# Optimization experiments

Measured on AMD Instinct MI355X. Metric: run time of the kernel, lower is better.

The kernel has to match this reference:

```python
import jax, jax.numpy as jnp
import numpy as np

M_DIM = 1024
N_HEADS = 16
H_DIM = M_DIM // N_HEADS
FFN_H = 2 * M_DIM
B, S = 2, 2048
EPS = 1e-5
NEG = -1e9


def layernorm(x, g, b):
    mu = jnp.mean(x, axis=-1, keepdims=True)
    var = jnp.mean((x - mu) ** 2, axis=-1, keepdims=True)
    return (x - mu) * jax.lax.rsqrt(var + EPS) * g + b


def setup_inputs() -> dict:
    key = jax.random.key(0)
    ks = jax.random.split(key, 16)
    sc = 0.02
    return {
        "x": jax.random.normal(ks[0], (B, S, M_DIM), jnp.float32),
        "attention_mask": jnp.ones((B, S), jnp.int32),
        # per-head QKV projections stacked over heads: [H, M, D]
        "Wq": jax.random.normal(ks[1], (N_HEADS, M_DIM, H_DIM), jnp.float32) * sc,
        "bq": jnp.zeros((N_HEADS, H_DIM), jnp.float32),
        "Wk": jax.random.normal(ks[2], (N_HEADS, M_DIM, H_DIM), jnp.float32) * sc,
        "bk": jnp.zeros((N_HEADS, H_DIM), jnp.float32),
        "Wv": jax.random.normal(ks[3], (N_HEADS, M_DIM, H_DIM), jnp.float32) * sc,
        "bv": jnp.zeros((N_HEADS, H_DIM), jnp.float32),
        "Wo": jax.random.normal(ks[4], (M_DIM, M_DIM), jnp.float32) * sc,
        "bo": jnp.zeros((M_DIM,), jnp.float32),
        "g1": jnp.ones((M_DIM,), jnp.float32),
        "b1": jnp.zeros((M_DIM,), jnp.float32),
        "W1": jax.random.normal(ks[5], (M_DIM, FFN_H), jnp.float32) * sc,
        "bias1": jnp.zeros((FFN_H,), jnp.float32),
        "W2": jax.random.normal(ks[6], (FFN_H, M_DIM), jnp.float32) * sc,
        "bias2": jnp.zeros((M_DIM,), jnp.float32),
        "g2": jnp.ones((M_DIM,), jnp.float32),
        "b2": jnp.zeros((M_DIM,), jnp.float32),
    }


def reference(x, attention_mask, Wq, bq, Wk, bk, Wv, bv, Wo, bo, g1, b1, W1, bias1, W2, bias2, g2, b2):
    # All heads at once (the torch code loops over heads; same math).
    q = jnp.einsum("bsm,hmd->bhsd", x, Wq) + bq[None, :, None, :]
    k = jnp.einsum("bsm,hmd->bhsd", x, Wk) + bk[None, :, None, :]
    v = jnp.einsum("bsm,hmd->bhsd", x, Wv) + bv[None, :, None, :]
    scores = jnp.einsum("bhqd,bhkd->bhqk", q, k) / jnp.sqrt(jnp.float32(H_DIM))
    mask = attention_mask[:, None, None, :].astype(bool)  # [B,1,1,S] over keys
    scores = jnp.where(mask, scores, NEG)
    attn = jax.nn.softmax(scores, axis=-1)
    ctx = jnp.einsum("bhqk,bhkd->bhqd", attn, v)
    ctx = ctx.transpose(0, 2, 1, 3).reshape(x.shape[0], x.shape[1], M_DIM)  # concat heads
    out = ctx @ Wo + bo
    out = layernorm(out + x, g1, b1)
    fout = jax.nn.relu(out @ W1 + bias1) @ W2 + bias2
    out = layernorm(out + fout, g2, b2)
    return out
```

## Files before the change

kernel.cpp:

```cpp
#include <hip/hip_runtime.h>

#define MDIM 1024
#define FFH  2048
#define SEQ  2048
#define AST  72
#define VST  136
#define QSCL 0.18033688f

#if __has_builtin(__builtin_amdgcn_exp2f)
  #define EXP2(x) __builtin_amdgcn_exp2f(x)
#else
  #define EXP2(x) exp2f(x)
#endif

typedef __attribute__((ext_vector_type(8))) __bf16 bf16x8;
typedef __attribute__((ext_vector_type(4))) float floatx4;
typedef __attribute__((ext_vector_type(8))) unsigned short ushort8;
typedef __attribute__((address_space(3))) unsigned int lds_uint;
typedef const __attribute__((address_space(1))) unsigned int g_uint;

__device__ __forceinline__ unsigned short f2bf(float f){
  union { float f; unsigned u; } v; v.f = f;
  unsigned u = v.u;
  u += 0x7fffu + ((u >> 16) & 1u);
  return (unsigned short)(u >> 16);
}
__device__ __forceinline__ unsigned short f2bf_tr(float f){
  union { float f; unsigned u; } v; v.f = f;
  return (unsigned short)(v.u >> 16);
}

__global__ void k_cvt_qb(const float* __restrict__ x, unsigned short* __restrict__ xb,
                         const float* __restrict__ bq, const float* __restrict__ bk,
                         const float* __restrict__ bv, float* __restrict__ qbias){
  const int bid = blockIdx.x, t = threadIdx.x;
  if (bid < 4096){
    int i = (bid * 256 + t) * 4;
    float4 v = *(const float4*)(x + i);
    ushort4 o;
    o.x = f2bf(v.x); o.y = f2bf(v.y); o.z = f2bf(v.z); o.w = f2bf(v.w);
    *(ushort4*)(xb + i) = o;
  } else {
    int i = (bid - 4096) * 256 + t;
    qbias[i] = (i < 1024) ? bq[i] * QSCL : (i < 2048) ? bk[i - 1024] : bv[i - 2048];
  }
}

__global__ void __launch_bounds__(256) k_prep_w(const float* __restrict__ Wo, const float* __restrict__ W1,
                                                const float* __restrict__ W2, const float* __restrict__ Wq,
                                                const float* __restrict__ Wk, const float* __restrict__ Wv,
                                                unsigned short* __restrict__ wot, unsigned short* __restrict__ w1t,
                                                unsigned short* __restrict__ w2t, unsigned short* __restrict__ wqkvt){
  __shared__ unsigned short Ts[32 * 36];
  const int t = threadIdx.x, bid = blockIdx.x;
  const int lr = t >> 3, lc4 = (t & 7) << 2;
  if (bid >= 5120){
    const int id = bid - 5120;
    const int xm = id & 31, yd = (id >> 5) & 1, z = id >> 6;
    const int tensor = z >> 4, h = z & 15;
    const float* W = (tensor == 0) ? Wq : (tensor == 1) ? Wk : Wv;
    const float scl = (tensor == 0) ? QSCL : 1.0f;
    const int m0 = xm << 5, d0 = yd << 5;
    float4 v = *(const float4*)(W + ((size_t)h << 16) + (size_t)(m0 + lr) * 64 + d0 + lc4);
    ushort4 o; o.x = f2bf(v.x * scl); o.y = f2bf(v.y * scl); o.z = f2bf(v.z * scl); o.w = f2bf(v.w * scl);
    *(ushort4*)&Ts[lr * 36 + lc4] = o;
    __syncthreads();
    ushort4 w;
    w.x = Ts[(lc4 + 0) * 36 + lr];
    w.y = Ts[(lc4 + 1) * 36 + lr];
    w.z = Ts[(lc4 + 2) * 36 + lr];
    w.w = Ts[(lc4 + 3) * 36 + lr];
    const int n = (tensor << 10) + (h << 6) + d0 + lr;
    *(ushort4*)(wqkvt + ((size_t)n << 10) + m0 + lc4) = w;
    return;
  }
  const float* src; unsigned short* dst; int K, N, k0, n0;
  if (bid < 1024){
    src = Wo; dst = wot; K = 1024; N = 1024;
    n0 = (bid & 31) << 5; k0 = (bid >> 5) << 5;
  } else if (bid < 3072){
    const int id = bid - 1024;
    src = W1; dst = w1t; K = 1024; N = 2048;
    n0 = (id & 63) << 5; k0 = (id >> 6) << 5;
  } else {
    const int id = bid - 3072;
    src = W2; dst = w2t; K = 2048; N = 1024;
    n0 = (id & 31) << 5; k0 = (id >> 5) << 5;
  }
  float4 v = *(const float4*)(src + (size_t)(k0 + lr) * N + n0 + lc4);
  ushort4 o; o.x = f2bf(v.x); o.y = f2bf(v.y); o.z = f2bf(v.z); o.w = f2bf(v.w);
  *(ushort4*)&Ts[lr * 36 + lc4] = o;
  __syncthreads();
  ushort4 w;
  w.x = Ts[(lc4 + 0) * 36 + lr];
  w.y = Ts[(lc4 + 1) * 36 + lr];
  w.z = Ts[(lc4 + 2) * 36 + lr];
  w.w = Ts[(lc4 + 3) * 36 + lr];
  *(ushort4*)(dst + (size_t)(n0 + lr) * K + k0 + lc4) = w;
}

template<int RELU, int OUTBF>
__global__ void __launch_bounds__(256) k_gemm128(const unsigned short* __restrict__ A,
                                                 const unsigned short* __restrict__ Bt,
                                                 const float* __restrict__ bias,
                                                 void* __restrict__ Cout, int N, int K){
  __shared__ unsigned short As[2][2 * 128 * 32];
  __shared__ unsigned short Bs[2][2 * 128 * 32];
  const int t = threadIdx.x;
  const int m0 = blockIdx.y << 7, n0 = blockIdx.x << 7;
  const int lane = t & 63, w = t >> 6;
  const int quad = lane >> 4, l16 = lane & 15;
  const int mw = (w & 1) << 6, nw = (w >> 1) << 6;
  floatx4 acc[4][4];
  #pragma unroll
  for (int i = 0; i < 4; i++)
    #pragma unroll
    for (int j = 0; j < 4; j++) acc[i][j] = (floatx4){0.f, 0.f, 0.f, 0.f};
  const unsigned short* Ag  = A  + (size_t)(m0 + (t >> 2)) * K + ((t & 3) << 3);
  const unsigned short* Ag2 = Ag + (size_t)64 * K;
  const unsigned short* Bg  = Bt + (size_t)(n0 + (t >> 2)) * K + ((t & 3) << 3);
  const unsigned short* Bg2 = Bg + (size_t)64 * K;

#define STG128(Ad, Bd, kb) { \
    _Pragma("unroll") \
    for (int s = 0; s < 2; s++){ \
      const int ko = (kb) + (s << 5), lo = (s << 12) + (t << 3); \
      __builtin_amdgcn_global_load_lds((g_uint*)(Ag  + ko), (lds_uint*)&(Ad)[lo],        16, 0, 0); \
      __builtin_amdgcn_global_load_lds((g_uint*)(Ag2 + ko), (lds_uint*)&(Ad)[lo + 2048], 16, 0, 0); \
      __builtin_amdgcn_global_load_lds((g_uint*)(Bg  + ko), (lds_uint*)&(Bd)[lo],        16, 0, 0); \
      __builtin_amdgcn_global_load_lds((g_uint*)(Bg2 + ko), (lds_uint*)&(Bd)[lo + 2048], 16, 0, 0); \
    } }

  STG128(As[0], Bs[0], 0);
  __syncthreads();
  int cur = 0;
  for (int kb = 0; kb < K; kb += 64){
    if (kb + 64 < K) STG128(As[cur ^ 1], Bs[cur ^ 1], kb + 64);
    const unsigned short* Ar = As[cur];
    const unsigned short* Br = Bs[cur];
    #pragma unroll
    for (int s = 0; s < 2; s++){
      const int sb = s << 12;
      bf16x8 af[4], bf[4];
      #pragma unroll
      for (int mt = 0; mt < 4; mt++)
        af[mt] = *(const bf16x8*)&Ar[sb + ((mw + (mt << 4) + l16) << 5) + (quad << 3)];
      #pragma unroll
      for (int nt = 0; nt < 4; nt++)
        bf[nt] = *(const bf16x8*)&Br[sb + ((nw + (nt << 4) + l16) << 5) + (quad << 3)];
      #pragma unroll
      for (int mt = 0; mt < 4; mt++)
        #pragma unroll
        for (int nt = 0; nt < 4; nt++)
          acc[mt][nt] = __builtin_amdgcn_mfma_f32_16x16x32_bf16(af[mt], bf[nt], acc[mt][nt], 0, 0, 0);
    }
    __syncthreads();
    cur ^= 1;
  }
#undef STG128
  #pragma unroll
  for (int nt = 0; nt < 4; nt++){
    const int col = n0 + nw + (nt << 4) + l16;
    const float bsv = bias[col];
    #pragma unroll
    for (int mt = 0; mt < 4; mt++){
      const int row = m0 + mw + (mt << 4) + (quad << 2);
      #pragma unroll
      for (int r = 0; r < 4; r++){
        float v = acc[mt][nt][r] + bsv;
        if (RELU) v = fmaxf(v, 0.f);
        if (OUTBF) ((unsigned short*)Cout)[(size_t)(row + r) * N + col] = f2bf(v);
        else       ((float*)Cout)[(size_t)(row + r) * N + col] = v;
      }
    }
  }
}

template<int RELU, int OUTBF>
__global__ void __launch_bounds__(256) k_gemm64n(const unsigned short* __restrict__ A,
                                                 const unsigned short* __restrict__ Bt,
                                                 const float* __restrict__ bias,
                                                 void* __restrict__ Cout, int N, int K){
  __shared__ unsigned short As[2][2 * 128 * 32];
  __shared__ unsigned short Bs[2][2 * 64 * 32];
  const int t = threadIdx.x;
  const int m0 = blockIdx.y << 7, n0 = blockIdx.x << 6;
  const int lane = t & 63, w = t >> 6;
  const int quad = lane >> 4, l16 = lane & 15;
  const int mw = (w & 1) << 6, nw = (w >> 1) << 5;
  floatx4 acc[4][2];
  #pragma unroll
  for (int i = 0; i < 4; i++)
    #pragma unroll
    for (int j = 0; j < 2; j++) acc[i][j] = (floatx4){0.f, 0.f, 0.f, 0.f};
  const unsigned short* Ag  = A  + (size_t)(m0 + (t >> 2)) * K + ((t & 3) << 3);
  const unsigned short* Ag2 = Ag + (size_t)64 * K;
  const unsigned short* Bg  = Bt + (size_t)(n0 + (t >> 2)) * K + ((t & 3) << 3);

#define STG64(Ad, Bd, kb) { \
    _Pragma("unroll") \
    for (int s = 0; s < 2; s++){ \
      const int ko = (kb) + (s << 5); \
      __builtin_amdgcn_global_load_lds((g_uint*)(Ag  + ko), (lds_uint*)&(Ad)[(s << 12) + (t << 3)],        16, 0, 0); \
      __builtin_amdgcn_global_load_lds((g_uint*)(Ag2 + ko), (lds_uint*)&(Ad)[(s << 12) + (t << 3) + 2048], 16, 0, 0); \
      __builtin_amdgcn_global_load_lds((g_uint*)(Bg  + ko), (lds_uint*)&(Bd)[(s << 11) + (t << 3)],        16, 0, 0); \
    } }

  STG64(As[0], Bs[0], 0);
  __syncthreads();
  int cur = 0;
  for (int kb = 0; kb < K; kb += 64){
    if (kb + 64 < K) STG64(As[cur ^ 1], Bs[cur ^ 1], kb + 64);
    const unsigned short* Ar = As[cur];
    const unsigned short* Br = Bs[cur];
    #pragma unroll
    for (int s = 0; s < 2; s++){
      bf16x8 af[4], bf[2];
      #pragma unroll
      for (int mt = 0; mt < 4; mt++)
        af[mt] = *(const bf16x8*)&Ar[(s << 12) + ((mw + (mt << 4) + l16) << 5) + (quad << 3)];
      #pragma unroll
      for (int nt = 0; nt < 2; nt++)
        bf[nt] = *(const bf16x8*)&Br[(s << 11) + ((nw + (nt << 4) + l16) << 5) + (quad << 3)];
      #pragma unroll
      for (int mt = 0; mt < 4; mt++)
        #pragma unroll
        for (int nt = 0; nt < 2; nt++)
          acc[mt][nt] = __builtin_amdgcn_mfma_f32_16x16x32_bf16(af[mt], bf[nt], acc[mt][nt], 0, 0, 0);
    }
    __syncthreads();
    cur ^= 1;
  }
#undef STG64
  #pragma unroll
  for (int nt = 0; nt < 2; nt++){
    const int col = n0 + nw + (nt << 4) + l16;
    const float bsv = bias[col];
    #pragma unroll
    for (int mt = 0; mt < 4; mt++){
      const int row = m0 + mw + (mt << 4) + (quad << 2);
      #pragma unroll
      for (int r = 0; r < 4; r++){
        float v = acc[mt][nt][r] + bsv;
        if (RELU) v = fmaxf(v, 0.f);
        if (OUTBF) ((unsigned short*)Cout)[(size_t)(row + r) * N + col] = f2bf(v);
        else       ((float*)Cout)[(size_t)(row + r) * N + col] = v;
      }
    }
  }
}

__global__ void __launch_bounds__(256, 2) k_attn(const unsigned short* __restrict__ qkvb,
                                                 const int* __restrict__ amask,
                                                 unsigned short* __restrict__ ctxb){
  __shared__ __align__(16) unsigned short Ks[2][128 * AST];
  __shared__ __align__(16) unsigned short Vt[2][64 * VST];
  __shared__ __align__(16) int msk[2][128];
  const int t = threadIdx.x;
  const int w = t >> 6, lane = t & 63;
  const int quad = lane >> 4, l16 = lane & 15;
  const int b = blockIdx.y >> 4, h = blockIdx.y & 15;
  const int q0 = blockIdx.x << 7;
  const int r0 = (w << 5) + l16;
  const int r1 = r0 + 16;
  const int sr = t >> 2, sc = (t & 3) << 4;
  const int kg = t >> 4, dc = (t & 15) << 2;
  const int swz  = (dc >> 4) & 3;
  const int pc0  = ((((kg & 3) | ((kg >> 3) << 2)) ^ swz) << 3) | (((kg >> 2) & 1) << 2);

  {
    const int qr = t >> 1, qc = (t & 1) << 5;
    const unsigned short* qs = qkvb + (size_t)((b << 11) + q0 + qr) * 3072 + (h << 6) + qc;
    unsigned short* qd = &Ks[0][qr * AST + qc];
    *(uint4*)(qd)      = *(const uint4*)(qs);
    *(uint4*)(qd + 8)  = *(const uint4*)(qs + 8);
    *(uint4*)(qd + 16) = *(const uint4*)(qs + 16);
    *(uint4*)(qd + 24) = *(const uint4*)(qs + 24);
  }
  __syncthreads();
  const bf16x8 qa0 = *(const bf16x8*)&Ks[0][r0 * AST + (quad << 3)];
  const bf16x8 qa1 = *(const bf16x8*)&Ks[0][r0 * AST + (quad << 3) + 32];
  const bf16x8 qb0 = *(const bf16x8*)&Ks[0][r1 * AST + (quad << 3)];
  const bf16x8 qb1 = *(const bf16x8*)&Ks[0][r1 * AST + (quad << 3) + 32];

  floatx4 accA[4], accB[4];
  #pragma unroll
  for (int i = 0; i < 4; i++){
    accA[i] = (floatx4){0.f, 0.f, 0.f, 0.f};
    accB[i] = (floatx4){0.f, 0.f, 0.f, 0.f};
  }
  float l_runA = 0.f, l_runB = 0.f;

  const unsigned short* kbase  = qkvb + (size_t)((b << 11) + sr) * 3072 + 1024 + (h << 6) + sc;
  const unsigned short* kbase2 = kbase + (size_t)64 * 3072;
  const unsigned short* vbase  = qkvb + (size_t)((b << 11) + (kg << 2)) * 3072 + 2048 + (h << 6) + dc;
  const unsigned short* vbase2 = vbase + (size_t)64 * 3072;
  const int* mbase = amask + (b << 11);

  uint4 krA, krB, krC, krD;
  ushort4 va0, va1, va2, va3, vb0, vb1, vb2, vb3;
  int mreg = 1;

#define LOADT(tt) { \
    const size_t off = (size_t)((tt) << 7) * 3072; \
    krA = *(const uint4*)(kbase + off); \
    krB = *(const uint4*)(kbase + off + 8); \
    krC = *(const uint4*)(kbase2 + off); \
    krD = *(const uint4*)(kbase2 + off + 8); \
    va0 = *(const ushort4*)(vbase + off); \
    va1 = *(const ushort4*)(vbase + off + 3072); \
    va2 = *(const ushort4*)(vbase + off + 2 * 3072); \
    va3 = *(const ushort4*)(vbase + off + 3 * 3072); \
    vb0 = *(const ushort4*)(vbase2 + off); \
    vb1 = *(const ushort4*)(vbase2 + off + 3072); \
    vb2 = *(const ushort4*)(vbase2 + off + 2 * 3072); \
    vb3 = *(const ushort4*)(vbase2 + off + 3 * 3072); \
    if (t < 128) mreg = mbase[((tt) << 7) + t]; \
  }

#define STORET(dst) { \
    unsigned short* Kd = Ks[dst]; \
    unsigned short* Vd = Vt[dst]; \
    *(uint4*)&Kd[sr * AST + sc]            = krA; \
    *(uint4*)&Kd[sr * AST + sc + 8]        = krB; \
    *(uint4*)&Kd[(sr + 64) * AST + sc]     = krC; \
    *(uint4*)&Kd[(sr + 64) * AST + sc + 8] = krD; \
    ushort4 cc; \
    cc.x = va0.x; cc.y = va1.x; cc.z = va2.x; cc.w = va3.x; *(ushort4*)&Vd[(dc + 0) * VST + pc0] = cc; \
    cc.x = va0.y; cc.y = va1.y; cc.z = va2.y; cc.w = va3.y; *(ushort4*)&Vd[(dc + 1) * VST + pc0] = cc; \
    cc.x = va0.z; cc.y = va1.z; cc.z = va2.z; cc.w = va3.z; *(ushort4*)&Vd[(dc + 2) * VST + pc0] = cc; \
    cc.x = va0.w; cc.y = va1.w; cc.z = va2.w; cc.w = va3.w; *(ushort4*)&Vd[(dc + 3) * VST + pc0] = cc; \
    cc.x = vb0.x; cc.y = vb1.x; cc.z = vb2.x; cc.w = vb3.x; *(ushort4*)&Vd[(dc + 0) * VST + pc0 + 64] = cc; \
    cc.x = vb0.y; cc.y = vb1.y; cc.z = vb2.y; cc.w = vb3.y; *(ushort4*)&Vd[(dc + 1) * VST + pc0 + 64] = cc; \
    cc.x = vb0.z; cc.y = vb1.z; cc.z = vb2.z; cc.w = vb3.z; *(ushort4*)&Vd[(dc + 2) * VST + pc0 + 64] = cc; \
    cc.x = vb0.w; cc.y = vb1.w; cc.z = vb2.w; cc.w = vb3.w; *(ushort4*)&Vd[(dc + 3) * VST + pc0 + 64] = cc; \
    if (t < 128) msk[dst][t] = mreg; \
  }

  LOADT(0);
  __syncthreads();
  STORET(0);
  LOADT(1);
  __syncthreads();

  int c = 0;
  for (int kt = 0; kt < 16; kt++){
    if (kt + 1 < 16) STORET(c ^ 1);
    if (kt + 2 < 16) LOADT(kt + 2);
    {
      const unsigned short* Kc = Ks[c];
      const unsigned short* Vc = Vt[c];
      const int* Mc = msk[c];
      float lsA = 0.f, lsB = 0.f;
      #pragma unroll
      for (int s = 0; s < 4; s++){
        const unsigned short* kp = &Kc[((s << 5) + l16) * AST + (quad << 3)];
        const bf16x8 k00 = *(const bf16x8*)(kp);
        const bf16x8 k01 = *(const bf16x8*)(kp + 32);
        const bf16x8 k10 = *(const bf16x8*)(kp + (AST << 4));
        const bf16x8 k11 = *(const bf16x8*)(kp + (AST << 4) + 32);
        floatx4 sA0 = (floatx4){0.f, 0.f, 0.f, 0.f};
        floatx4 sB0 = (floatx4){0.f, 0.f, 0.f, 0.f};
        floatx4 sA1 = (floatx4){0.f, 0.f, 0.f, 0.f};
        floatx4 sB1 = (floatx4){0.f, 0.f, 0.f, 0.f};
        __builtin_amdgcn_s_setprio(1);
        sA0 = __builtin_amdgcn_mfma_f32_16x16x32_bf16(k00, qa0, sA0, 0, 0, 0);
        sA0 = __builtin_amdgcn_mfma_f32_16x16x32_bf16(k01, qa1, sA0, 0, 0, 0);
        sB0 = __builtin_amdgcn_mfma_f32_16x16x32_bf16(k00, qb0, sB0, 0, 0, 0);
        sB0 = __builtin_amdgcn_mfma_f32_16x16x32_bf16(k01, qb1, sB0, 0, 0, 0);
        sA1 = __builtin_amdgcn_mfma_f32_16x16x32_bf16(k10, qa0, sA1, 0, 0, 0);
        sA1 = __builtin_amdgcn_mfma_f32_16x16x32_bf16(k11, qa1, sA1, 0, 0, 0);
        sB1 = __builtin_amdgcn_mfma_f32_16x16x32_bf16(k10, qb0, sB1, 0, 0, 0);
        sB1 = __builtin_amdgcn_mfma_f32_16x16x32_bf16(k11, qb1, sB1, 0, 0, 0);
        __builtin_amdgcn_s_setprio(0);
        const int4 m0 = *(const int4*)&Mc[(s << 5) + (quad << 2)];
        const int4 m1 = *(const int4*)&Mc[(s << 5) + 16 + (quad << 2)];
        const float a0 = m0.x ? EXP2(sA0[0]) : 0.f;
        const float a1 = m0.y ? EXP2(sA0[1]) : 0.f;
        const float a2 = m0.z ? EXP2(sA0[2]) : 0.f;
        const float a3 = m0.w ? EXP2(sA0[3]) : 0.f;
        const float a4 = m1.x ? EXP2(sA1[0]) : 0.f;
        const float a5 = m1.y ? EXP2(sA1[1]) : 0.f;
        const float a6 = m1.z ? EXP2(sA1[2]) : 0.f;
        const float a7 = m1.w ? EXP2(sA1[3]) : 0.f;
        const float b0 = m0.x ? EXP2(sB0[0]) : 0.f;
        const float b1 = m0.y ? EXP2(sB0[1]) : 0.f;
        const float b2 = m0.z ? EXP2(sB0[2]) : 0.f;
        const float b3 = m0.w ? EXP2(sB0[3]) : 0.f;
        const float b4 = m1.x ? EXP2(sB1[0]) : 0.f;
        const float b5 = m1.y ? EXP2(sB1[1]) : 0.f;
        const float b6 = m1.z ? EXP2(sB1[2]) : 0.f;
        const float b7 = m1.w ? EXP2(sB1[3]) : 0.f;
        lsA += (a0 + a1) + (a2 + a3) + (a4 + a5) + (a6 + a7);
        lsB += (b0 + b1) + (b2 + b3) + (b4 + b5) + (b6 + b7);
        ushort8 uA, uB;
        uA[0] = f2bf_tr(a0); uA[1] = f2bf_tr(a1); uA[2] = f2bf_tr(a2); uA[3] = f2bf_tr(a3);
        uA[4] = f2bf_tr(a4); uA[5] = f2bf_tr(a5); uA[6] = f2bf_tr(a6); uA[7] = f2bf_tr(a7);
        uB[0] = f2bf_tr(b0); uB[1] = f2bf_tr(b1); uB[2] = f2bf_tr(b2); uB[3] = f2bf_tr(b3);
        uB[4] = f2bf_tr(b4); uB[5] = f2bf_tr(b5); uB[6] = f2bf_tr(b6); uB[7] = f2bf_tr(b7);
        const bf16x8 pfA = __builtin_bit_cast(bf16x8, uA);
        const bf16x8 pfB = __builtin_bit_cast(bf16x8, uB);
        __builtin_amdgcn_s_setprio(1);
        #pragma unroll
        for (int mt = 0; mt < 4; mt++){
          const bf16x8 vf = *(const bf16x8*)&Vc[((mt << 4) + l16) * VST + ((((s << 2) + quad) ^ mt) << 3)];
          accA[mt] = __builtin_amdgcn_mfma_f32_16x16x32_bf16(vf, pfA, accA[mt], 0, 0, 0);
          accB[mt] = __builtin_amdgcn_mfma_f32_16x16x32_bf16(vf, pfB, accB[mt], 0, 0, 0);
        }
        __builtin_amdgcn_s_setprio(0);
      }
      l_runA += lsA;
      l_runB += lsB;
    }
    __syncthreads();
    c ^= 1;
  }
#undef LOADT
#undef STORET

  l_runA += __shfl_xor(l_runA, 16);
  l_runA += __shfl_xor(l_runA, 32);
  l_runB += __shfl_xor(l_runB, 16);
  l_runB += __shfl_xor(l_runB, 32);
  const float liA = 1.f / l_runA;
  const float liB = 1.f / l_runB;
  unsigned short* oA = ctxb + (size_t)((b << 11) + q0 + r0) * 1024 + (h << 6);
  unsigned short* oB = ctxb + (size_t)((b << 11) + q0 + r1) * 1024 + (h << 6);
  #pragma unroll
  for (int mt = 0; mt < 4; mt++){
    ushort4 o;
    o.x = f2bf(accA[mt][0] * liA);
    o.y = f2bf(accA[mt][1] * liA);
    o.z = f2bf(accA[mt][2] * liA);
    o.w = f2bf(accA[mt][3] * liA);
    *(ushort4*)&oA[(mt << 4) + (quad << 2)] = o;
    o.x = f2bf(accB[mt][0] * liB);
    o.y = f2bf(accB[mt][1] * liB);
    o.z = f2bf(accB[mt][2] * liB);
    o.w = f2bf(accB[mt][3] * liB);
    *(ushort4*)&oB[(mt << 4) + (quad << 2)] = o;
  }
}

__global__ void __launch_bounds__(256) k_ln(const unsigned short* __restrict__ a,
                                            const float* __restrict__ res,
                                            const float* __restrict__ gg, const float* __restrict__ bb,
                                            float* __restrict__ out, unsigned short* __restrict__ outb){
  const int row = blockIdx.x, t = threadIdx.x;
  const ushort4 au = ((const ushort4*)(a + (size_t)row * 1024))[t];
  const float4 rv = ((const float4*)(res + (size_t)row * 1024))[t];
  float4 v;
  { union { unsigned u; float f; } c;
    c.u = (unsigned)au.x << 16; v.x = c.f + rv.x;
    c.u = (unsigned)au.y << 16; v.y = c.f + rv.y;
    c.u = (unsigned)au.z << 16; v.z = c.f + rv.z;
    c.u = (unsigned)au.w << 16; v.w = c.f + rv.w; }
  float sum = v.x + v.y + v.z + v.w;
  float ss  = v.x * v.x + v.y * v.y + v.z * v.z + v.w * v.w;
  #pragma unroll
  for (int off = 32; off > 0; off >>= 1){
    sum += __shfl_down(sum, off);
    ss  += __shfl_down(ss, off);
  }
  __shared__ float red[8];
  const int w = t >> 6;
  if ((t & 63) == 0){ red[w] = sum; red[4 + w] = ss; }
  __syncthreads();
  const float S  = red[0] + red[1] + red[2] + red[3];
  const float SS = red[4] + red[5] + red[6] + red[7];
  const float mu  = S * (1.f / 1024.f);
  const float var = SS * (1.f / 1024.f) - mu * mu;
  const float rs  = rsqrtf(var + 1e-5f);
  const float4 gv = ((const float4*)gg)[t];
  const float4 bv = ((const float4*)bb)[t];
  float4 o;
  o.x = (v.x - mu) * rs * gv.x + bv.x;
  o.y = (v.y - mu) * rs * gv.y + bv.y;
  o.z = (v.z - mu) * rs * gv.z + bv.z;
  o.w = (v.w - mu) * rs * gv.w + bv.w;
  ((float4*)(out + (size_t)row * 1024))[t] = o;
  if (outb){
    ushort4 ob; ob.x = f2bf(o.x); ob.y = f2bf(o.y); ob.z = f2bf(o.z); ob.w = f2bf(o.w);
    ((ushort4*)(outb + (size_t)row * 1024))[t] = ob;
  }
}

extern "C" void kernel_launch(void* const* d_in, const int* in_sizes, int n_in,
                              void* d_out, int out_size, void* d_ws, size_t ws_size,
                              hipStream_t stream){
  const float* x     = (const float*)d_in[0];
  const int*   amask = (const int*)d_in[1];
  const float* Wq    = (const float*)d_in[2];
  const float* bq    = (const float*)d_in[3];
  const float* Wk    = (const float*)d_in[4];
  const float* bk    = (const float*)d_in[5];
  const float* Wv    = (const float*)d_in[6];
  const float* bv    = (const float*)d_in[7];
  const float* Wo    = (const float*)d_in[8];
  const float* bo    = (const float*)d_in[9];
  const float* g1    = (const float*)d_in[10];
  const float* b1    = (const float*)d_in[11];
  const float* W1    = (const float*)d_in[12];
  const float* bias1 = (const float*)d_in[13];
  const float* W2    = (const float*)d_in[14];
  const float* bias2 = (const float*)d_in[15];
  const float* g2    = (const float*)d_in[16];
  const float* b2    = (const float*)d_in[17];

  char* ws = (char*)d_ws;
  unsigned short* xb    = (unsigned short*)(ws + 0);
  unsigned short* wqkvt = (unsigned short*)(ws + 8388608);
  float*          qbias = (float*)         (ws + 14680064);
  unsigned short* wot   = (unsigned short*)(ws + 14692352);
  unsigned short* w1t   = (unsigned short*)(ws + 16789504);
  unsigned short* w2t   = (unsigned short*)(ws + 20983808);
  unsigned short* ctxb  = (unsigned short*)(ws + 25178112);
  unsigned short* attnb = (unsigned short*)(ws + 33566720);
  unsigned short* fbufb = attnb;
  unsigned short* qkvb  = (unsigned short*)(ws + 50343936);
  float*          out1  = (float*)         (ws + 50343936);
  unsigned short* out1b = (unsigned short*)(ws + 50343936 + 25165824);
  unsigned short* h1    = (unsigned short*)(ws + 50343936 + 33554432);

  k_cvt_qb<<<dim3(4108), dim3(256), 0, stream>>>(x, xb, bq, bk, bv, qbias);
  k_prep_w<<<dim3(8192), dim3(256), 0, stream>>>(Wo, W1, W2, Wq, Wk, Wv, wot, w1t, w2t, wqkvt);

  k_gemm128<0,1><<<dim3(24, 32), dim3(256), 0, stream>>>(xb, wqkvt, qbias, qkvb, 3072, 1024);
  k_attn<<<dim3(16, 32), dim3(256), 0, stream>>>(qkvb, amask, ctxb);
  k_gemm64n<0,1><<<dim3(16, 32), dim3(256), 0, stream>>>(ctxb, wot, bo, attnb, MDIM, 1024);
  k_ln<<<dim3(4096), dim3(256), 0, stream>>>(attnb, x, g1, b1, out1, out1b);
  k_gemm128<1,1><<<dim3(16, 32), dim3(256), 0, stream>>>(out1b, w1t, bias1, h1, FFH, 1024);
  k_gemm64n<0,1><<<dim3(16, 32), dim3(256), 0, stream>>>(h1, w2t, bias2, fbufb, MDIM, 2048);
  k_ln<<<dim3(4096), dim3(256), 0, stream>>>(fbufb, out1, g2, b2, (float*)d_out, nullptr);
}
```

Measured before the change: 303.8 us.

## Halve GEMM K-tile for higher occupancy and remap attention blocks per XCD

The 128x128 GEMM now stages a 32-wide K slice per buffer instead of 64, which halves LDS use and lets the kernel request three blocks per CU via launch bounds. The cost is twice as many barriers and loop iterations. The attention kernel also remaps the linear block index so that all query tiles of a given batch-head land on the same XCD, which is meant to improve L2 reuse of the K/V tiles. The remap is a bijection over the 512 blocks, so the same work is still covered.

```diff
diff --git a/kernel.cpp b/kernel.cpp
--- a/kernel.cpp
+++ b/kernel.cpp
@@ -100,12 +100,12 @@
 }
 
 template<int RELU, int OUTBF>
-__global__ void __launch_bounds__(256) k_gemm128(const unsigned short* __restrict__ A,
+__global__ void __launch_bounds__(256, 3) k_gemm128(const unsigned short* __restrict__ A,
                                                  const unsigned short* __restrict__ Bt,
                                                  const float* __restrict__ bias,
                                                  void* __restrict__ Cout, int N, int K){
-  __shared__ unsigned short As[2][2 * 128 * 32];
-  __shared__ unsigned short Bs[2][2 * 128 * 32];
+  __shared__ unsigned short As[2][128 * 32];
+  __shared__ unsigned short Bs[2][128 * 32];
   const int t = threadIdx.x;
   const int m0 = blockIdx.y << 7, n0 = blockIdx.x << 7;
   const int lane = t & 63, w = t >> 6;
@@ -122,38 +122,31 @@
   const unsigned short* Bg2 = Bg + (size_t)64 * K;
 
 #define STG128(Ad, Bd, kb) { \
-    _Pragma("unroll") \
-    for (int s = 0; s < 2; s++){ \
-      const int ko = (kb) + (s << 5), lo = (s << 12) + (t << 3); \
-      __builtin_amdgcn_global_load_lds((g_uint*)(Ag  + ko), (lds_uint*)&(Ad)[lo],        16, 0, 0); \
-      __builtin_amdgcn_global_load_lds((g_uint*)(Ag2 + ko), (lds_uint*)&(Ad)[lo + 2048], 16, 0, 0); \
-      __builtin_amdgcn_global_load_lds((g_uint*)(Bg  + ko), (lds_uint*)&(Bd)[lo],        16, 0, 0); \
-      __builtin_amdgcn_global_load_lds((g_uint*)(Bg2 + ko), (lds_uint*)&(Bd)[lo + 2048], 16, 0, 0); \
-    } }
+    __builtin_amdgcn_global_load_lds((g_uint*)(Ag  + (kb)), (lds_uint*)&(Ad)[t << 3],          16, 0, 0); \
+    __builtin_amdgcn_global_load_lds((g_uint*)(Ag2 + (kb)), (lds_uint*)&(Ad)[(t << 3) + 2048], 16, 0, 0); \
+    __builtin_amdgcn_global_load_lds((g_uint*)(Bg  + (kb)), (lds_uint*)&(Bd)[t << 3],          16, 0, 0); \
+    __builtin_amdgcn_global_load_lds((g_uint*)(Bg2 + (kb)), (lds_uint*)&(Bd)[(t << 3) + 2048], 16, 0, 0); \
+  }
 
   STG128(As[0], Bs[0], 0);
   __syncthreads();
   int cur = 0;
-  for (int kb = 0; kb < K; kb += 64){
-    if (kb + 64 < K) STG128(As[cur ^ 1], Bs[cur ^ 1], kb + 64);
+  for (int kb = 0; kb < K; kb += 32){
+    if (kb + 32 < K) STG128(As[cur ^ 1], Bs[cur ^ 1], kb + 32);
     const unsigned short* Ar = As[cur];
     const unsigned short* Br = Bs[cur];
-    #pragma unroll
-    for (int s = 0; s < 2; s++){
-      const int sb = s << 12;
-      bf16x8 af[4], bf[4];
-      #pragma unroll
-      for (int mt = 0; mt < 4; mt++)
-        af[mt] = *(const bf16x8*)&Ar[sb + ((mw + (mt << 4) + l16) << 5) + (quad << 3)];
+    bf16x8 af[4], bf[4];
+    #pragma unroll
+    for (int mt = 0; mt < 4; mt++)
+      af[mt] = *(const bf16x8*)&Ar[((mw + (mt << 4) + l16) << 5) + (quad << 3)];
+    #pragma unroll
+    for (int nt = 0; nt < 4; nt++)
+      bf[nt] = *(const bf16x8*)&Br[((nw + (nt << 4) + l16) << 5) + (quad << 3)];
+    #pragma unroll
+    for (int mt = 0; mt < 4; mt++)
       #pragma unroll
       for (int nt = 0; nt < 4; nt++)
-        bf[nt] = *(const bf16x8*)&Br[sb + ((nw + (nt << 4) + l16) << 5) + (quad << 3)];
-      #pragma unroll
-      for (int mt = 0; mt < 4; mt++)
-        #pragma unroll
-        for (int nt = 0; nt < 4; nt++)
-          acc[mt][nt] = __builtin_amdgcn_mfma_f32_16x16x32_bf16(af[mt], bf[nt], acc[mt][nt], 0, 0, 0);
-    }
+        acc[mt][nt] = __builtin_amdgcn_mfma_f32_16x16x32_bf16(af[mt], bf[nt], acc[mt][nt], 0, 0, 0);
     __syncthreads();
     cur ^= 1;
   }
@@ -259,8 +252,11 @@
   const int t = threadIdx.x;
   const int w = t >> 6, lane = t & 63;
   const int quad = lane >> 4, l16 = lane & 15;
-  const int b = blockIdx.y >> 4, h = blockIdx.y & 15;
-  const int q0 = blockIdx.x << 7;
+  const int lin = (blockIdx.y << 4) | blockIdx.x;
+  const int xcd = lin & 7, jj = lin >> 3;
+  const int bh = (xcd << 2) | (jj >> 4);
+  const int b = bh >> 4, h = bh & 15;
+  const int q0 = (jj & 15) << 7;
   const int r0 = (w << 5) + l16;
   const int r1 = r0 + 16;
   const int sr = t >> 2, sc = (t & 3) << 4;
```

Result: faster. 297.2 us (-2.2%).
